# Kernel optimization log

Hardware: AMD Instinct MI355X
Metric: run time of the kernel (lower is better)

Reference implementation:

```python
import jax, jax.numpy as jnp
import numpy as np

DIM = 2048
N_HEADS = 16
HEAD_DIM = DIM // N_HEADS
MAX_SEQ_LEN = 2048
THRESHOLD = 0.7
LN_EPS = 1e-5


def _layernorm(x, g, b):
    mu = jnp.mean(x, axis=-1, keepdims=True)
    var = jnp.mean(jnp.square(x - mu), axis=-1, keepdims=True)
    return (x - mu) * jax.lax.rsqrt(var + LN_EPS) * g + b


def _act_quant(x):
    # 8-bit absmax activation quantization (per-tensor), straight-through
    s = 127.0 / jnp.maximum(jnp.max(jnp.abs(x)), 1e-5)
    xq = jnp.clip(jnp.round(x * s), -128.0, 127.0) / s
    return x + jax.lax.stop_gradient(xq - x)


def _ternary_quant(w):
    # W1.58 ternary: zero weights below threshold*mean|w|, scale = mean |w| over survivors
    delta = THRESHOLD * jnp.mean(jnp.abs(w))
    mask = (jnp.abs(w) > delta).astype(w.dtype)
    alpha = jnp.sum(jnp.abs(w) * mask) / jnp.maximum(jnp.sum(mask), 1.0)
    wq = jnp.sign(w) * mask * alpha
    return w + jax.lax.stop_gradient(wq - w)


def _bitlinear(x, w, g, b):
    x = _layernorm(x, g, b)
    xq = _act_quant(x)
    wq = _ternary_quant(w)
    return xq @ wq.T


def _rope_tables():
    inv = 1.0 / (10000.0 ** (np.arange(0, HEAD_DIM, 2, dtype=np.float32) / HEAD_DIM))
    t = np.arange(MAX_SEQ_LEN, dtype=np.float32)
    ang = np.outer(t, inv)  # (max_seq, head_dim/2)
    return jnp.asarray(np.cos(ang)), jnp.asarray(np.sin(ang))


def _apply_rope(x, cos_t, sin_t):
    # Faithful to source: x is (B, H, S, D) and freqs are indexed by x.shape[1] == H
    n = x.shape[1]
    xr = x.reshape(*x.shape[:-1], HEAD_DIM // 2, 2)
    a, b = xr[..., 0], xr[..., 1]
    c = cos_t[:n][None, :, None, :]  # (1, H, 1, D/2)
    s = sin_t[:n][None, :, None, :]
    out = jnp.stack([a * c - b * s, a * s + b * c], axis=-1)
    return out.reshape(x.shape)


def setup_inputs() -> dict:
    key = jax.random.key(0)
    ks = jax.random.split(key, 5)
    std = np.sqrt(2.0 / DIM)
    d = {"x": jax.random.normal(ks[0], (2, MAX_SEQ_LEN, DIM), dtype=jnp.float32)}
    for i, nm in enumerate(["q", "k", "v", "o"]):
        d[f"w_{nm}"] = jax.random.normal(ks[i + 1], (DIM, DIM), dtype=jnp.float32) * std
        d[f"g_{nm}"] = jnp.ones((DIM,), dtype=jnp.float32)
        d[f"b_{nm}"] = jnp.zeros((DIM,), dtype=jnp.float32)
    return d


def reference(x, w_q, g_q, b_q, w_k, g_k, b_k, w_v, g_v, b_v, w_o, g_o, b_o):
    B, S, _ = x.shape
    cos_t, sin_t = _rope_tables()
    scale = HEAD_DIM ** -0.5

    def split_heads(t):
        return t.reshape(B, S, N_HEADS, HEAD_DIM).transpose(0, 2, 1, 3)

    q = split_heads(_bitlinear(x, w_q, g_q, b_q))
    k = split_heads(_bitlinear(x, w_k, g_k, b_k))
    v = split_heads(_bitlinear(x, w_v, g_v, b_v))
    q = _apply_rope(q, cos_t, sin_t)
    k = _apply_rope(k, cos_t, sin_t)
    scores = jnp.einsum("bhsd,bhtd->bhst", q, k) * scale
    attn = jax.nn.softmax(scores, axis=-1)
    out = jnp.einsum("bhst,bhtd->bhsd", attn, v)
    out = out.transpose(0, 2, 1, 3).reshape(B, S, DIM)
    return _bitlinear(out, w_o, g_o, b_o)
```

## Files before the change

### kernel.cpp

```cpp
#include <hip/hip_runtime.h>
#include <math.h>

#define DIM 2048
#define NROWS 4096
#define WN (DIM*DIM)
#define HEADS 16
#define HDIM 128
#define SEQ 2048

typedef __attribute__((ext_vector_type(8))) short short8;
typedef __attribute__((ext_vector_type(8))) _Float16 half8;
typedef __attribute__((ext_vector_type(4))) float floatx4;
typedef __attribute__((ext_vector_type(4))) int intx4;

__device__ __forceinline__ unsigned short f2h(float f) {
  _Float16 h = (_Float16)f;
  return __builtin_bit_cast(unsigned short, h);
}
__device__ __forceinline__ float h2f(unsigned short u) {
  _Float16 h = __builtin_bit_cast(_Float16, u);
  return (float)h;
}

__device__ __forceinline__ void gload_lds16(const void* g, void* l) {
  __builtin_amdgcn_global_load_lds(
      (const __attribute__((address_space(1))) unsigned int*)g,
      (__attribute__((address_space(3))) unsigned int*)l, 16, 0, 0);
}

__device__ __forceinline__ float wredSum(float v) {
  #pragma unroll
  for (int o = 1; o < 64; o <<= 1) v += __shfl_xor(v, o);
  return v;
}
__device__ __forceinline__ float wredMax(float v) {
  #pragma unroll
  for (int o = 1; o < 64; o <<= 1) v = fmaxf(v, __shfl_xor(v, o));
  return v;
}

__device__ __forceinline__ float blockReduceSum(float v, float* red) {
  int tid = threadIdx.x;
  red[tid] = v; __syncthreads();
  for (int s = 128; s > 0; s >>= 1) {
    if (tid < s) red[tid] += red[tid + s];
    __syncthreads();
  }
  float r = red[0]; __syncthreads();
  return r;
}

__device__ __forceinline__ const float* pick_w(const float* a, const float* b,
                                               const float* c, const float* d, int i) {
  return i == 0 ? a : i == 1 ? b : i == 2 ? c : d;
}

__global__ __launch_bounds__(256) void w_abs_partial(
    const float* w0, const float* w1, const float* w2, const float* w3, float* part)
{
  const float4* w4 = (const float4*)pick_w(w0, w1, w2, w3, blockIdx.y);
  float s = 0.f;
  for (int i = blockIdx.x * 256 + threadIdx.x; i < WN / 4; i += 1024 * 256) {
    float4 v = w4[i];
    s += fabsf(v.x) + fabsf(v.y) + fabsf(v.z) + fabsf(v.w);
  }
  __shared__ float red[256];
  float t = blockReduceSum(s, red);
  if (threadIdx.x == 0) part[blockIdx.y * 1024 + blockIdx.x] = t;
}

__global__ __launch_bounds__(256) void w_delta_final(const float* part, float* stats)
{
  float s = 0.f;
  for (int i = threadIdx.x; i < 1024; i += 256) s += part[blockIdx.x * 1024 + i];
  __shared__ float red[256];
  float t = blockReduceSum(s, red);
  if (threadIdx.x == 0) stats[blockIdx.x] = 0.7f * (t / (float)WN);
}

__device__ __forceinline__ signed char tq(float v, float delta) {
  if (fabsf(v) > delta) return (v > 0.f) ? (signed char)1 : (signed char)-1;
  return (signed char)0;
}

__global__ __launch_bounds__(256) void w_maskquant(
    const float* w0, const float* w1, const float* w2, const float* w3,
    const float* stats, float* part2, signed char* tern)
{
  int wi = blockIdx.y;
  const float4* w4 = (const float4*)pick_w(w0, w1, w2, w3, wi);
  float delta = stats[wi];
  char4* out = (char4*)(tern + (size_t)wi * WN);
  float s = 0.f, cnt = 0.f;
  for (int i = blockIdx.x * 256 + threadIdx.x; i < WN / 4; i += 1024 * 256) {
    float4 v = w4[i];
    char4 o;
    float a;
    a = fabsf(v.x); if (a > delta) { s += a; cnt += 1.f; } o.x = tq(v.x, delta);
    a = fabsf(v.y); if (a > delta) { s += a; cnt += 1.f; } o.y = tq(v.y, delta);
    a = fabsf(v.z); if (a > delta) { s += a; cnt += 1.f; } o.z = tq(v.z, delta);
    a = fabsf(v.w); if (a > delta) { s += a; cnt += 1.f; } o.w = tq(v.w, delta);
    out[i] = o;
  }
  __shared__ float red[256];
  float ts = blockReduceSum(s, red);
  float tc = blockReduceSum(cnt, red);
  if (threadIdx.x == 0) {
    part2[((size_t)blockIdx.y * 1024 + blockIdx.x) * 2]     = ts;
    part2[((size_t)blockIdx.y * 1024 + blockIdx.x) * 2 + 1] = tc;
  }
}

__global__ __launch_bounds__(256) void w_alpha_final(const float* part2, float* stats)
{
  float s = 0.f, c = 0.f;
  for (int i = threadIdx.x; i < 1024; i += 256) {
    s += part2[((size_t)blockIdx.x * 1024 + i) * 2];
    c += part2[((size_t)blockIdx.x * 1024 + i) * 2 + 1];
  }
  __shared__ float red[256];
  float ts = blockReduceSum(s, red);
  float tc = blockReduceSum(c, red);
  if (threadIdx.x == 0) stats[4 + blockIdx.x] = ts / fmaxf(tc, 1.f);
}

__global__ __launch_bounds__(256) void ln_absmax3(
    const float* __restrict__ x,
    const float* __restrict__ g0, const float* __restrict__ b0,
    const float* __restrict__ g1, const float* __restrict__ b1,
    const float* __restrict__ g2, const float* __restrict__ b2,
    float* __restrict__ pmax)
{
  const int lane = threadIdx.x & 63;
  const int row = blockIdx.x * 4 + (threadIdx.x >> 6);
  const float* xr = x + (size_t)row * DIM;
  float4 a[8];
  float s = 0.f, sq = 0.f;
  #pragma unroll
  for (int j = 0; j < 8; ++j) {
    a[j] = *(const float4*)(xr + j * 256 + lane * 4);
    s  += a[j].x + a[j].y + a[j].z + a[j].w;
    sq += a[j].x*a[j].x + a[j].y*a[j].y + a[j].z*a[j].z + a[j].w*a[j].w;
  }
  s = wredSum(s); sq = wredSum(sq);
  float mu = s * (1.f / DIM);
  float var = sq * (1.f / DIM) - mu * mu;
  float rstd = 1.f / sqrtf(var + 1e-5f);
  const float* gs[3] = {g0, g1, g2};
  const float* bs[3] = {b0, b1, b2};
  #pragma unroll
  for (int p = 0; p < 3; ++p) {
    float m = 0.f;
    #pragma unroll
    for (int j = 0; j < 8; ++j) {
      float4 gg = *(const float4*)(gs[p] + j * 256 + lane * 4);
      float4 bb = *(const float4*)(bs[p] + j * 256 + lane * 4);
      m = fmaxf(m, fabsf((a[j].x - mu) * rstd * gg.x + bb.x));
      m = fmaxf(m, fabsf((a[j].y - mu) * rstd * gg.y + bb.y));
      m = fmaxf(m, fabsf((a[j].z - mu) * rstd * gg.z + bb.z));
      m = fmaxf(m, fabsf((a[j].w - mu) * rstd * gg.w + bb.w));
    }
    m = wredMax(m);
    if (lane == 0) pmax[(size_t)p * NROWS + row] = m;
  }
}

__global__ __launch_bounds__(256) void absmax_final(
    const float* __restrict__ pmax, unsigned* __restrict__ ambits)
{
  const float* src = pmax + (size_t)blockIdx.x * NROWS;
  float m = 0.f;
  for (int i = threadIdx.x; i < NROWS; i += 256) m = fmaxf(m, src[i]);
  m = wredMax(m);
  __shared__ float red[4];
  if ((threadIdx.x & 63) == 0) red[threadIdx.x >> 6] = m;
  __syncthreads();
  if (threadIdx.x == 0)
    ambits[blockIdx.x] = __float_as_uint(fmaxf(fmaxf(red[0], red[1]), fmaxf(red[2], red[3])));
}

__global__ __launch_bounds__(256) void ln_quant3(
    const float* __restrict__ x,
    const float* __restrict__ g0, const float* __restrict__ b0,
    const float* __restrict__ g1, const float* __restrict__ b1,
    const float* __restrict__ g2, const float* __restrict__ b2,
    const unsigned* __restrict__ ambits,
    signed char* __restrict__ xq0, signed char* __restrict__ xq1,
    signed char* __restrict__ xq2)
{
  const int lane = threadIdx.x & 63;
  const int row = blockIdx.x * 4 + (threadIdx.x >> 6);
  const float* xr = x + (size_t)row * DIM;
  float4 a[8];
  float s = 0.f, sq = 0.f;
  #pragma unroll
  for (int j = 0; j < 8; ++j) {
    a[j] = *(const float4*)(xr + j * 256 + lane * 4);
    s  += a[j].x + a[j].y + a[j].z + a[j].w;
    sq += a[j].x*a[j].x + a[j].y*a[j].y + a[j].z*a[j].z + a[j].w*a[j].w;
  }
  s = wredSum(s); sq = wredSum(sq);
  float mu = s * (1.f / DIM);
  float var = sq * (1.f / DIM) - mu * mu;
  float rstd = 1.f / sqrtf(var + 1e-5f);
  const float* gs[3] = {g0, g1, g2};
  const float* bs[3] = {b0, b1, b2};
  signed char* outs[3] = {xq0, xq1, xq2};
  #pragma unroll
  for (int p = 0; p < 3; ++p) {
    float sc = 127.f / fmaxf(__uint_as_float(ambits[p]), 1e-5f);
    #pragma unroll
    for (int j = 0; j < 8; ++j) {
      float4 gg = *(const float4*)(gs[p] + j * 256 + lane * 4);
      float4 bb = *(const float4*)(bs[p] + j * 256 + lane * 4);
      float y0 = (a[j].x - mu) * rstd * gg.x + bb.x;
      float y1 = (a[j].y - mu) * rstd * gg.y + bb.y;
      float y2 = (a[j].z - mu) * rstd * gg.z + bb.z;
      float y3 = (a[j].w - mu) * rstd * gg.w + bb.w;
      char4 q;
      q.x = (signed char)(int)fminf(fmaxf(rintf(y0 * sc), -128.f), 127.f);
      q.y = (signed char)(int)fminf(fmaxf(rintf(y1 * sc), -128.f), 127.f);
      q.z = (signed char)(int)fminf(fmaxf(rintf(y2 * sc), -128.f), 127.f);
      q.w = (signed char)(int)fminf(fmaxf(rintf(y3 * sc), -128.f), 127.f);
      *(char4*)(outs[p] + (size_t)row * DIM + j * 256 + lane * 4) = q;
    }
  }
}

template<int MODE>
__global__ __launch_bounds__(256) void ln_kernel(
    const float* __restrict__ x, const float* __restrict__ g, const float* __restrict__ bias,
    const unsigned* __restrict__ ambits, float* __restrict__ pmax,
    signed char* __restrict__ xq)
{
  const int lane = threadIdx.x & 63;
  const int row = blockIdx.x * 4 + (threadIdx.x >> 6);
  const float* xr = x + (size_t)row * DIM;
  float4 a[8];
  float s = 0.f, sq = 0.f;
  #pragma unroll
  for (int j = 0; j < 8; ++j) {
    a[j] = *(const float4*)(xr + j * 256 + lane * 4);
    s  += a[j].x + a[j].y + a[j].z + a[j].w;
    sq += a[j].x*a[j].x + a[j].y*a[j].y + a[j].z*a[j].z + a[j].w*a[j].w;
  }
  s = wredSum(s); sq = wredSum(sq);
  float mu = s * (1.f / DIM);
  float var = sq * (1.f / DIM) - mu * mu;
  float rstd = 1.f / sqrtf(var + 1e-5f);
  if (MODE == 0) {
    float m = 0.f;
    #pragma unroll
    for (int j = 0; j < 8; ++j) {
      float4 gg = *(const float4*)(g + j * 256 + lane * 4);
      float4 bb = *(const float4*)(bias + j * 256 + lane * 4);
      m = fmaxf(m, fabsf((a[j].x - mu) * rstd * gg.x + bb.x));
      m = fmaxf(m, fabsf((a[j].y - mu) * rstd * gg.y + bb.y));
      m = fmaxf(m, fabsf((a[j].z - mu) * rstd * gg.z + bb.z));
      m = fmaxf(m, fabsf((a[j].w - mu) * rstd * gg.w + bb.w));
    }
    m = wredMax(m);
    if (lane == 0) pmax[row] = m;
  } else {
    float sc = 127.f / fmaxf(__uint_as_float(*ambits), 1e-5f);
    #pragma unroll
    for (int j = 0; j < 8; ++j) {
      float4 gg = *(const float4*)(g + j * 256 + lane * 4);
      float4 bb = *(const float4*)(bias + j * 256 + lane * 4);
      float y0 = (a[j].x - mu) * rstd * gg.x + bb.x;
      float y1 = (a[j].y - mu) * rstd * gg.y + bb.y;
      float y2 = (a[j].z - mu) * rstd * gg.z + bb.z;
      float y3 = (a[j].w - mu) * rstd * gg.w + bb.w;
      char4 q;
      q.x = (signed char)(int)fminf(fmaxf(rintf(y0 * sc), -128.f), 127.f);
      q.y = (signed char)(int)fminf(fmaxf(rintf(y1 * sc), -128.f), 127.f);
      q.z = (signed char)(int)fminf(fmaxf(rintf(y2 * sc), -128.f), 127.f);
      q.w = (signed char)(int)fminf(fmaxf(rintf(y3 * sc), -128.f), 127.f);
      *(char4*)(xq + (size_t)row * DIM + j * 256 + lane * 4) = q;
    }
  }
}

__global__ __launch_bounds__(256) void gemm_qkv(
    const signed char* __restrict__ A0, const signed char* __restrict__ A1,
    const signed char* __restrict__ A2, const signed char* __restrict__ Bt0,
    unsigned short* __restrict__ C0, unsigned short* __restrict__ C1,
    unsigned short* __restrict__ C2t, const float* __restrict__ stats)
{
  const int tid = threadIdx.x;
  const int lane = tid & 63;
  const int w = tid >> 6;
  const int wm = w >> 1, wn = w & 1;
  const int quad = lane >> 4, l16 = lane & 15;
  const int bm = blockIdx.x * 128, bn = blockIdx.y * 128;
  const int z = blockIdx.z;

  const signed char* A  = z == 0 ? A0 : z == 1 ? A1 : A2;
  const signed char* Bt = Bt0 + (size_t)z * WN;

  __shared__ __align__(16) signed char smem[2 * 128 * 128];
  signed char* As = smem;
  signed char* Bs = smem + 128 * 128;

  const int srow_off = lane >> 3;
  const int scol     = (lane & 7) * 16;

  intx4 acc[4][4];
  #pragma unroll
  for (int i = 0; i < 4; ++i)
    #pragma unroll
    for (int j = 0; j < 4; ++j) acc[i][j] = {0, 0, 0, 0};

  for (int k0 = 0; k0 < DIM; k0 += 128) {
    #pragma unroll
    for (int i = 0; i < 4; ++i) {
      int c = i * 4 + w;
      int row = c * 8 + srow_off;
      gload_lds16(A  + (size_t)(bm + row) * DIM + k0 + scol, &As[c * 1024]);
      gload_lds16(Bt + (size_t)(bn + row) * DIM + k0 + scol, &Bs[c * 1024]);
    }
    __syncthreads();
    #pragma unroll
    for (int kc = 0; kc < 2; ++kc) {
      intx4 af[4], bf[4];
      #pragma unroll
      for (int i = 0; i < 4; ++i)
        af[i] = *(const intx4*)&As[(wm * 64 + i * 16 + l16) * 128 + kc * 64 + quad * 16];
      #pragma unroll
      for (int j = 0; j < 4; ++j)
        bf[j] = *(const intx4*)&Bs[(wn * 64 + j * 16 + l16) * 128 + kc * 64 + quad * 16];
      #pragma unroll
      for (int i = 0; i < 4; ++i)
        #pragma unroll
        for (int j = 0; j < 4; ++j)
          acc[i][j] = __builtin_amdgcn_mfma_i32_16x16x64_i8(af[i], bf[j], acc[i][j], 0, 0, 0);
    }
    __syncthreads();
  }

  const unsigned* am = (const unsigned*)(stats + 8);
  float scale = stats[4 + z] * fmaxf(__uint_as_float(am[z]), 1e-5f) * (1.f / 127.f);

  if (z < 2) {
    unsigned short* Cp = z == 0 ? C0 : C1;
    #pragma unroll
    for (int i = 0; i < 4; ++i)
      #pragma unroll
      for (int j = 0; j < 4; ++j)
        #pragma unroll
        for (int r = 0; r < 4; ++r) {
          int m = bm + wm * 64 + i * 16 + quad * 4 + r;
          int n = bn + wn * 64 + j * 16 + l16;
          Cp[(size_t)m * DIM + n] = f2h((float)acc[i][j][r] * scale);
        }
  } else {
    #pragma unroll
    for (int i = 0; i < 4; ++i)
      #pragma unroll
      for (int j = 0; j < 4; ++j)
        #pragma unroll
        for (int r = 0; r < 4; ++r) {
          int s = wm * 64 + i * 16 + quad * 4 + r;
          int d = wn * 64 + j * 16 + l16;
          int byte = (d * 256 + s * 2) ^ ((d & 7) << 4);
          *(unsigned short*)(smem + byte) = f2h((float)acc[i][j][r] * scale);
        }
    __syncthreads();
    const int b = bm >> 11;
    const int s_base = bm & (SEQ - 1);
    const int h = blockIdx.y;
    const int sc = (tid & 15) * 8;
    #pragma unroll
    for (int pass = 0; pass < 8; ++pass) {
      int d = (tid >> 4) + pass * 16;
      int byte = (d * 256 + sc * 2) ^ ((d & 7) << 4);
      *(uint4*)(C2t + ((size_t)(b * HEADS + h) * HDIM + d) * SEQ + s_base + sc) =
          *(const uint4*)(smem + byte);
    }
  }
}

__global__ __launch_bounds__(256) void gemm_bt(
    const signed char* __restrict__ A, const signed char* __restrict__ Bt,
    float* __restrict__ Cp, const float* __restrict__ stats, int wi)
{
  const int tid = threadIdx.x;
  const int lane = tid & 63;
  const int w = tid >> 6;
  const int wm = w >> 1, wn = w & 1;
  const int quad = lane >> 4, l16 = lane & 15;
  const int bm = blockIdx.x * 128, bn = blockIdx.y * 128;

  __shared__ __align__(16) signed char As[128 * 128];
  __shared__ __align__(16) signed char Bs[128 * 128];

  const int srow_off = lane >> 3;
  const int scol     = (lane & 7) * 16;

  intx4 acc[4][4];
  #pragma unroll
  for (int i = 0; i < 4; ++i)
    #pragma unroll
    for (int j = 0; j < 4; ++j) acc[i][j] = {0, 0, 0, 0};

  for (int k0 = 0; k0 < DIM; k0 += 128) {
    #pragma unroll
    for (int i = 0; i < 4; ++i) {
      int c = i * 4 + w;
      int row = c * 8 + srow_off;
      gload_lds16(A  + (size_t)(bm + row) * DIM + k0 + scol, &As[c * 1024]);
      gload_lds16(Bt + (size_t)(bn + row) * DIM + k0 + scol, &Bs[c * 1024]);
    }
    __syncthreads();
    #pragma unroll
    for (int kc = 0; kc < 2; ++kc) {
      intx4 af[4], bf[4];
      #pragma unroll
      for (int i = 0; i < 4; ++i)
        af[i] = *(const intx4*)&As[(wm * 64 + i * 16 + l16) * 128 + kc * 64 + quad * 16];
      #pragma unroll
      for (int j = 0; j < 4; ++j)
        bf[j] = *(const intx4*)&Bs[(wn * 64 + j * 16 + l16) * 128 + kc * 64 + quad * 16];
      #pragma unroll
      for (int i = 0; i < 4; ++i)
        #pragma unroll
        for (int j = 0; j < 4; ++j)
          acc[i][j] = __builtin_amdgcn_mfma_i32_16x16x64_i8(af[i], bf[j], acc[i][j], 0, 0, 0);
    }
    __syncthreads();
  }

  const unsigned* am = (const unsigned*)(stats + 8);
  float scale = stats[4 + wi] * fmaxf(__uint_as_float(am[wi]), 1e-5f) * (1.f / 127.f);
  #pragma unroll
  for (int i = 0; i < 4; ++i)
    #pragma unroll
    for (int j = 0; j < 4; ++j)
      #pragma unroll
      for (int r = 0; r < 4; ++r) {
        int m = bm + wm * 64 + i * 16 + quad * 4 + r;
        int n = bn + wn * 64 + j * 16 + l16;
        Cp[(size_t)m * DIM + n] = (float)acc[i][j][r] * scale;
      }
}

__global__ __launch_bounds__(256) void rope_kernel(unsigned short* q, unsigned short* k)
{
  const float SC = 0.12751741769011063f;
  int idx = blockIdx.x * 256 + threadIdx.x;
  int p = idx & 63;
  int h = (idx >> 6) & (HEADS - 1);
  int r = idx >> 10;
  float inv = exp2f((float)p * -0.20762050593046f);
  float ang = (float)h * inv;
  float sn, cs;
  __sincosf(ang, &sn, &cs);
  size_t base = (size_t)r * DIM + h * HDIM + 2 * p;
  {
    float a = h2f(q[base]), b = h2f(q[base + 1]);
    q[base]     = f2h((a * cs - b * sn) * SC);
    q[base + 1] = f2h((a * sn + b * cs) * SC);
  }
  {
    float a = h2f(k[base]), b = h2f(k[base + 1]);
    k[base]     = f2h(a * cs - b * sn);
    k[base + 1] = f2h(a * sn + b * cs);
  }
}

__global__ __launch_bounds__(256, 4) void flash_attn(
    const unsigned short* __restrict__ qf, const unsigned short* __restrict__ kf,
    const unsigned short* __restrict__ vt, float* __restrict__ o)
{
  const int tid = threadIdx.x;
  const int lane = tid & 63;
  const int w = tid >> 6;
  const int quad = lane >> 4;
  const int l16 = lane & 15;
  const int L = blockIdx.x;
  const int slot = L >> 3;
  const int bh = ((L & 7) << 2) | (slot >> 5);
  const int qt = slot & 31;
  const int b = bh >> 4;
  const int h = bh & 15;

  __shared__ __align__(16) char Ks[64 * 256];
  __shared__ __align__(16) char Vs[128 * 128];
  __shared__ __align__(16) char Ps[4][16 * 128];

  const size_t qbase = ((size_t)(b * SEQ + qt * 64 + w * 16 + l16)) * DIM + h * HDIM;
  short8 qa[4];
  #pragma unroll
  for (int kc = 0; kc < 4; ++kc)
    qa[kc] = *(const short8*)(qf + qbase + kc * 32 + quad * 8);

  float m_q = -INFINITY;
  float l_q = 0.f;
  floatx4 accO[8];
  #pragma unroll
  for (int i = 0; i < 8; ++i) accO[i] = {0.f, 0.f, 0.f, 0.f};

  const char* kg = (const char*)(kf + (size_t)(b * SEQ) * DIM + h * HDIM);
  const char* vg = (const char*)(vt + (size_t)bh * HDIM * SEQ);

  int koff[4], voff[4];
  #pragma unroll
  for (int j = 0; j < 4; ++j) {
    int c = w * 4 + j;
    int rK = c * 4 + (lane >> 4);
    koff[j] = rK * (DIM * 2) + (((lane & 15) * 16) ^ ((rK & 7) << 4));
    int rV = c * 8 + (lane >> 3);
    voff[j] = rV * (SEQ * 2) + (((lane & 7) * 16) ^ ((rV & 7) << 4));
  }

  for (int kt = 0; kt < SEQ / 64; ++kt) {
    __syncthreads();
    const char* kgb = kg + (size_t)kt * 64 * DIM * 2;
    const char* vgb = vg + (size_t)kt * 128;
    #pragma unroll
    for (int j = 0; j < 4; ++j) {
      int c = w * 4 + j;
      gload_lds16(kgb + koff[j], &Ks[c * 1024]);
      gload_lds16(vgb + voff[j], &Vs[c * 1024]);
    }
    asm volatile("s_waitcnt vmcnt(0)" ::: "memory");
    __syncthreads();

    float sreg[4][4];
    __builtin_amdgcn_s_setprio(1);
    #pragma unroll
    for (int jt = 0; jt < 4; ++jt) {
      floatx4 a0 = {0.f, 0.f, 0.f, 0.f};
      #pragma unroll
      for (int kc = 0; kc < 4; ++kc) {
        int kr = jt * 16 + l16;
        short8 kb = *(const short8*)&Ks[(kr * 256 + kc * 64 + quad * 16) ^ ((kr & 7) << 4)];
        a0 = __builtin_amdgcn_mfma_f32_16x16x32_f16(
            __builtin_bit_cast(half8, kb), __builtin_bit_cast(half8, qa[kc]), a0, 0, 0, 0);
      }
      #pragma unroll
      for (int r = 0; r < 4; ++r) sreg[jt][r] = a0[r];
    }
    __builtin_amdgcn_s_setprio(0);

    float mx = sreg[0][0];
    #pragma unroll
    for (int jt = 0; jt < 4; ++jt)
      #pragma unroll
      for (int r = 0; r < 4; ++r) mx = fmaxf(mx, sreg[jt][r]);
    mx = fmaxf(mx, __shfl_xor(mx, 16));
    mx = fmaxf(mx, __shfl_xor(mx, 32));
    int need = !__all(mx <= m_q + 8.f);
    float mnew, alpha;
    if (need) {
      mnew = fmaxf(m_q, mx);
      alpha = exp2f(m_q - mnew);
      m_q = mnew;
    } else {
      mnew = m_q;
      alpha = 1.f;
    }
    float ssum = 0.f;
    #pragma unroll
    for (int jt = 0; jt < 4; ++jt) {
      ushort4 pk;
      float p0 = exp2f(sreg[jt][0] - mnew);
      float p1 = exp2f(sreg[jt][1] - mnew);
      float p2 = exp2f(sreg[jt][2] - mnew);
      float p3 = exp2f(sreg[jt][3] - mnew);
      pk.x = f2h(p0); pk.y = f2h(p1); pk.z = f2h(p2); pk.w = f2h(p3);
      ssum += (p0 + p1) + (p2 + p3);
      *(ushort4*)&Ps[w][(l16 * 128 + jt * 32 + quad * 8) ^ ((l16 & 7) << 4)] = pk;
    }
    ssum += __shfl_xor(ssum, 16);
    ssum += __shfl_xor(ssum, 32);
    l_q = l_q * alpha + ssum;
    if (need) {
      #pragma unroll
      for (int dt = 0; dt < 8; ++dt)
        #pragma unroll
        for (int r = 0; r < 4; ++r) accO[dt][r] *= alpha;
    }

    __builtin_amdgcn_s_setprio(1);
    #pragma unroll
    for (int kc = 0; kc < 2; ++kc) {
      short8 pf = *(const short8*)&Ps[w][(l16 * 128 + kc * 64 + quad * 16) ^ ((l16 & 7) << 4)];
      #pragma unroll
      for (int dt = 0; dt < 8; ++dt) {
        int vr = dt * 16 + l16;
        short8 vf = *(const short8*)&Vs[(vr * 128 + kc * 64 + quad * 16) ^ ((vr & 7) << 4)];
        accO[dt] = __builtin_amdgcn_mfma_f32_16x16x32_f16(
            __builtin_bit_cast(half8, vf), __builtin_bit_cast(half8, pf), accO[dt], 0, 0, 0);
      }
    }
    __builtin_amdgcn_s_setprio(0);
  }

  float invl = 1.0f / l_q;
  const size_t obase = (size_t)(b * SEQ + qt * 64 + w * 16 + l16) * DIM + h * HDIM;
  #pragma unroll
  for (int dt = 0; dt < 8; ++dt) {
    float4 ov;
    ov.x = accO[dt][0] * invl; ov.y = accO[dt][1] * invl;
    ov.z = accO[dt][2] * invl; ov.w = accO[dt][3] * invl;
    *(float4*)(o + obase + dt * 16 + quad * 4) = ov;
  }
}

extern "C" void kernel_launch(void* const* d_in, const int* in_sizes, int n_in,
                              void* d_out, int out_size, void* d_ws, size_t ws_size,
                              hipStream_t stream)
{
  (void)in_sizes; (void)n_in; (void)out_size; (void)ws_size;
  const float* x = (const float*)d_in[0];
  const float* w[4]; const float* g[4]; const float* bb[4];
  for (int i = 0; i < 4; ++i) {
    w[i]  = (const float*)d_in[1 + 3 * i];
    g[i]  = (const float*)d_in[2 + 3 * i];
    bb[i] = (const float*)d_in[3 + 3 * i];
  }

  char* base = (char*)d_ws;
  size_t off = 0;
  auto alloc = [&](size_t bytes) {
    char* p = base + off;
    off += (bytes + 255) & ~(size_t)255;
    return p;
  };
  const size_t ACTH = (size_t)NROWS * DIM * 2;
  const size_t ACT8 = (size_t)NROWS * DIM;
  float* stats          = (float*)alloc(64);
  float* part1          = (float*)alloc(4 * 1024 * sizeof(float));
  float* part2          = (float*)alloc(4 * 1024 * 2 * sizeof(float));
  float* pmax           = (float*)alloc((size_t)4 * NROWS * sizeof(float));
  signed char* tern     = (signed char*)alloc((size_t)4 * WN);
  signed char* xq0      = (signed char*)alloc(ACT8);
  signed char* xq1      = (signed char*)alloc(ACT8);
  signed char* xq2      = (signed char*)alloc(ACT8);
  unsigned short* qh    = (unsigned short*)alloc(ACTH);
  unsigned short* kh    = (unsigned short*)alloc(ACTH);
  unsigned short* vtb   = (unsigned short*)alloc(ACTH);
  float* oat            = (float*)alloc((size_t)NROWS * DIM * sizeof(float));
  signed char* xqo = xq0;
  unsigned* ambits = (unsigned*)(stats + 8);

  hipMemsetAsync(stats, 0, 64, stream);

  dim3 b256(256);
  w_abs_partial<<<dim3(1024, 4), b256, 0, stream>>>(w[0], w[1], w[2], w[3], part1);
  w_delta_final<<<4, b256, 0, stream>>>(part1, stats);
  w_maskquant<<<dim3(1024, 4), b256, 0, stream>>>(w[0], w[1], w[2], w[3], stats, part2, tern);
  w_alpha_final<<<4, b256, 0, stream>>>(part2, stats);

  ln_absmax3<<<NROWS / 4, b256, 0, stream>>>(x, g[0], bb[0], g[1], bb[1], g[2], bb[2], pmax);
  absmax_final<<<3, b256, 0, stream>>>(pmax, ambits);
  ln_quant3<<<NROWS / 4, b256, 0, stream>>>(x, g[0], bb[0], g[1], bb[1], g[2], bb[2], ambits,
                                            xq0, xq1, xq2);

  gemm_qkv<<<dim3(NROWS / 128, DIM / 128, 3), b256, 0, stream>>>(
      xq0, xq1, xq2, tern, qh, kh, vtb, stats);

  rope_kernel<<<NROWS * 1024 / 256, b256, 0, stream>>>(qh, kh);
  flash_attn<<<dim3(32 * 32), b256, 0, stream>>>(qh, kh, vtb, oat);

  ln_kernel<0><<<NROWS / 4, b256, 0, stream>>>(oat, g[3], bb[3], nullptr,
                                               pmax + (size_t)3 * NROWS, nullptr);
  absmax_final<<<1, b256, 0, stream>>>(pmax + (size_t)3 * NROWS, ambits + 3);
  ln_kernel<1><<<NROWS / 4, b256, 0, stream>>>(oat, g[3], bb[3], ambits + 3, nullptr, xqo);
  gemm_bt<<<dim3(NROWS / 128, DIM / 128), b256, 0, stream>>>(
      xqo, tern + (size_t)3 * WN, (float*)d_out, stats, 3);
}
```

Before: 442.6 us.

## Double query rows per flash-attention wave to reuse K/V tiles

Each wave now processes two 16-row query fragments (128 query rows per block), so every K and V fragment loaded from LDS feeds two MFMAs. The grid shrinks to 512 blocks and launch bounds drop to 2 blocks per CU to make room for the doubled accumulators and score registers. P is packed to fp16 with the packed round-toward-zero convert. The aim is to halve K/V global and LDS traffic per query row, at the cost of lower occupancy and fewer blocks to spread across the GPU.

```diff
diff --git a/kernel.cpp b/kernel.cpp
--- a/kernel.cpp
+++ b/kernel.cpp
@@ -20,6 +20,9 @@
 __device__ __forceinline__ float h2f(unsigned short u) {
   _Float16 h = __builtin_bit_cast(_Float16, u);
   return (float)h;
+}
+__device__ __forceinline__ unsigned pkh2(float a, float b) {
+  return __builtin_bit_cast(unsigned, __builtin_amdgcn_cvt_pkrtz(a, b));
 }
 
 __device__ __forceinline__ void gload_lds16(const void* g, void* l) {
@@ -468,7 +471,7 @@
   }
 }
 
-__global__ __launch_bounds__(256, 4) void flash_attn(
+__global__ __launch_bounds__(256, 2) void flash_attn(
     const unsigned short* __restrict__ qf, const unsigned short* __restrict__ kf,
     const unsigned short* __restrict__ vt, float* __restrict__ o)
 {
@@ -479,26 +482,28 @@
   const int l16 = lane & 15;
   const int L = blockIdx.x;
   const int slot = L >> 3;
-  const int bh = ((L & 7) << 2) | (slot >> 5);
-  const int qt = slot & 31;
+  const int bh = ((L & 7) << 2) | (slot >> 4);
+  const int qt = slot & 15;
   const int b = bh >> 4;
   const int h = bh & 15;
 
   __shared__ __align__(16) char Ks[64 * 256];
   __shared__ __align__(16) char Vs[128 * 128];
-  __shared__ __align__(16) char Ps[4][16 * 128];
-
-  const size_t qbase = ((size_t)(b * SEQ + qt * 64 + w * 16 + l16)) * DIM + h * HDIM;
-  short8 qa[4];
-  #pragma unroll
-  for (int kc = 0; kc < 4; ++kc)
-    qa[kc] = *(const short8*)(qf + qbase + kc * 32 + quad * 8);
-
-  float m_q = -INFINITY;
-  float l_q = 0.f;
-  floatx4 accO[8];
-  #pragma unroll
-  for (int i = 0; i < 8; ++i) accO[i] = {0.f, 0.f, 0.f, 0.f};
+  __shared__ __align__(16) char Ps[4][32 * 128];
+
+  const size_t qbase = ((size_t)(b * SEQ + qt * 128 + w * 32 + l16)) * DIM + h * HDIM;
+  short8 qa[2][4];
+  #pragma unroll
+  for (int f = 0; f < 2; ++f)
+    #pragma unroll
+    for (int kc = 0; kc < 4; ++kc)
+      qa[f][kc] = *(const short8*)(qf + qbase + (size_t)f * 16 * DIM + kc * 32 + quad * 8);
+
+  float m_q[2] = {-INFINITY, -INFINITY};
+  float l_q[2] = {0.f, 0.f};
+  floatx4 accO0[8], accO1[8];
+  #pragma unroll
+  for (int i = 0; i < 8; ++i) { accO0[i] = {0.f, 0.f, 0.f, 0.f}; accO1[i] = {0.f, 0.f, 0.f, 0.f}; }
 
   const char* kg = (const char*)(kf + (size_t)(b * SEQ) * DIM + h * HDIM);
   const char* vg = (const char*)(vt + (size_t)bh * HDIM * SEQ);
@@ -526,85 +531,105 @@
     asm volatile("s_waitcnt vmcnt(0)" ::: "memory");
     __syncthreads();
 
-    float sreg[4][4];
+    float sreg[2][4][4];
     __builtin_amdgcn_s_setprio(1);
     #pragma unroll
     for (int jt = 0; jt < 4; ++jt) {
-      floatx4 a0 = {0.f, 0.f, 0.f, 0.f};
+      floatx4 a0 = {0.f, 0.f, 0.f, 0.f}, a1 = {0.f, 0.f, 0.f, 0.f};
       #pragma unroll
       for (int kc = 0; kc < 4; ++kc) {
         int kr = jt * 16 + l16;
         short8 kb = *(const short8*)&Ks[(kr * 256 + kc * 64 + quad * 16) ^ ((kr & 7) << 4)];
         a0 = __builtin_amdgcn_mfma_f32_16x16x32_f16(
-            __builtin_bit_cast(half8, kb), __builtin_bit_cast(half8, qa[kc]), a0, 0, 0, 0);
+            __builtin_bit_cast(half8, kb), __builtin_bit_cast(half8, qa[0][kc]), a0, 0, 0, 0);
+        a1 = __builtin_amdgcn_mfma_f32_16x16x32_f16(
+            __builtin_bit_cast(half8, kb), __builtin_bit_cast(half8, qa[1][kc]), a1, 0, 0, 0);
       }
       #pragma unroll
-      for (int r = 0; r < 4; ++r) sreg[jt][r] = a0[r];
+      for (int r = 0; r < 4; ++r) { sreg[0][jt][r] = a0[r]; sreg[1][jt][r] = a1[r]; }
     }
     __builtin_amdgcn_s_setprio(0);
 
-    float mx = sreg[0][0];
-    #pragma unroll
-    for (int jt = 0; jt < 4; ++jt)
-      #pragma unroll
-      for (int r = 0; r < 4; ++r) mx = fmaxf(mx, sreg[jt][r]);
-    mx = fmaxf(mx, __shfl_xor(mx, 16));
-    mx = fmaxf(mx, __shfl_xor(mx, 32));
-    int need = !__all(mx <= m_q + 8.f);
-    float mnew, alpha;
-    if (need) {
-      mnew = fmaxf(m_q, mx);
-      alpha = exp2f(m_q - mnew);
-      m_q = mnew;
-    } else {
-      mnew = m_q;
-      alpha = 1.f;
-    }
-    float ssum = 0.f;
-    #pragma unroll
-    for (int jt = 0; jt < 4; ++jt) {
-      ushort4 pk;
-      float p0 = exp2f(sreg[jt][0] - mnew);
-      float p1 = exp2f(sreg[jt][1] - mnew);
-      float p2 = exp2f(sreg[jt][2] - mnew);
-      float p3 = exp2f(sreg[jt][3] - mnew);
-      pk.x = f2h(p0); pk.y = f2h(p1); pk.z = f2h(p2); pk.w = f2h(p3);
-      ssum += (p0 + p1) + (p2 + p3);
-      *(ushort4*)&Ps[w][(l16 * 128 + jt * 32 + quad * 8) ^ ((l16 & 7) << 4)] = pk;
-    }
-    ssum += __shfl_xor(ssum, 16);
-    ssum += __shfl_xor(ssum, 32);
-    l_q = l_q * alpha + ssum;
-    if (need) {
+    float alpha[2]; int need[2];
+    #pragma unroll
+    for (int f = 0; f < 2; ++f) {
+      float mx = sreg[f][0][0];
+      #pragma unroll
+      for (int jt = 0; jt < 4; ++jt)
+        #pragma unroll
+        for (int r = 0; r < 4; ++r) mx = fmaxf(mx, sreg[f][jt][r]);
+      mx = fmaxf(mx, __shfl_xor(mx, 16));
+      mx = fmaxf(mx, __shfl_xor(mx, 32));
+      need[f] = !__all(mx <= m_q[f] + 8.f);
+      float mnew;
+      if (need[f]) {
+        mnew = fmaxf(m_q[f], mx);
+        alpha[f] = exp2f(m_q[f] - mnew);
+        m_q[f] = mnew;
+      } else {
+        mnew = m_q[f];
+        alpha[f] = 1.f;
+      }
+      float ssum = 0.f;
+      #pragma unroll
+      for (int jt = 0; jt < 4; ++jt) {
+        float p0 = exp2f(sreg[f][jt][0] - mnew);
+        float p1 = exp2f(sreg[f][jt][1] - mnew);
+        float p2 = exp2f(sreg[f][jt][2] - mnew);
+        float p3 = exp2f(sreg[f][jt][3] - mnew);
+        uint2 pk2;
+        pk2.x = pkh2(p0, p1);
+        pk2.y = pkh2(p2, p3);
+        ssum += (p0 + p1) + (p2 + p3);
+        *(uint2*)&Ps[w][((f * 16 + l16) * 128 + jt * 32 + quad * 8) ^ ((l16 & 7) << 4)] = pk2;
+      }
+      ssum += __shfl_xor(ssum, 16);
+      ssum += __shfl_xor(ssum, 32);
+      l_q[f] = l_q[f] * alpha[f] + ssum;
+    }
+    if (need[0]) {
       #pragma unroll
       for (int dt = 0; dt < 8; ++dt)
         #pragma unroll
-        for (int r = 0; r < 4; ++r) accO[dt][r] *= alpha;
+        for (int r = 0; r < 4; ++r) accO0[dt][r] *= alpha[0];
+    }
+    if (need[1]) {
+      #pragma unroll
+      for (int dt = 0; dt < 8; ++dt)
+        #pragma unroll
+        for (int r = 0; r < 4; ++r) accO1[dt][r] *= alpha[1];
     }
 
     __builtin_amdgcn_s_setprio(1);
     #pragma unroll
     for (int kc = 0; kc < 2; ++kc) {
-      short8 pf = *(const short8*)&Ps[w][(l16 * 128 + kc * 64 + quad * 16) ^ ((l16 & 7) << 4)];
+      short8 pf0 = *(const short8*)&Ps[w][(l16 * 128 + kc * 64 + quad * 16) ^ ((l16 & 7) << 4)];
+      short8 pf1 = *(const short8*)&Ps[w][((16 + l16) * 128 + kc * 64 + quad * 16) ^ ((l16 & 7) << 4)];
       #pragma unroll
       for (int dt = 0; dt < 8; ++dt) {
         int vr = dt * 16 + l16;
         short8 vf = *(const short8*)&Vs[(vr * 128 + kc * 64 + quad * 16) ^ ((vr & 7) << 4)];
-        accO[dt] = __builtin_amdgcn_mfma_f32_16x16x32_f16(
-            __builtin_bit_cast(half8, vf), __builtin_bit_cast(half8, pf), accO[dt], 0, 0, 0);
+        accO0[dt] = __builtin_amdgcn_mfma_f32_16x16x32_f16(
+            __builtin_bit_cast(half8, vf), __builtin_bit_cast(half8, pf0), accO0[dt], 0, 0, 0);
+        accO1[dt] = __builtin_amdgcn_mfma_f32_16x16x32_f16(
+            __builtin_bit_cast(half8, vf), __builtin_bit_cast(half8, pf1), accO1[dt], 0, 0, 0);
       }
     }
     __builtin_amdgcn_s_setprio(0);
   }
 
-  float invl = 1.0f / l_q;
-  const size_t obase = (size_t)(b * SEQ + qt * 64 + w * 16 + l16) * DIM + h * HDIM;
-  #pragma unroll
-  for (int dt = 0; dt < 8; ++dt) {
-    float4 ov;
-    ov.x = accO[dt][0] * invl; ov.y = accO[dt][1] * invl;
-    ov.z = accO[dt][2] * invl; ov.w = accO[dt][3] * invl;
-    *(float4*)(o + obase + dt * 16 + quad * 4) = ov;
+  #pragma unroll
+  for (int f = 0; f < 2; ++f) {
+    float invl = 1.0f / l_q[f];
+    const size_t obase = (size_t)(b * SEQ + qt * 128 + w * 32 + f * 16 + l16) * DIM + h * HDIM;
+    #pragma unroll
+    for (int dt = 0; dt < 8; ++dt) {
+      floatx4 acc = f == 0 ? accO0[dt] : accO1[dt];
+      float4 ov;
+      ov.x = acc[0] * invl; ov.y = acc[1] * invl;
+      ov.z = acc[2] * invl; ov.w = acc[3] * invl;
+      *(float4*)(o + obase + dt * 16 + quad * 4) = ov;
+    }
   }
 }
 
@@ -662,7 +687,7 @@
       xq0, xq1, xq2, tern, qh, kh, vtb, stats);
 
   rope_kernel<<<NROWS * 1024 / 256, b256, 0, stream>>>(qh, kh);
-  flash_attn<<<dim3(32 * 32), b256, 0, stream>>>(qh, kh, vtb, oat);
+  flash_attn<<<dim3(16 * 32), b256, 0, stream>>>(qh, kh, vtb, oat);
 
   ln_kernel<0><<<NROWS / 4, b256, 0, stream>>>(oat, g[3], bb[3], nullptr,
                                                pmax + (size_t)3 * NROWS, nullptr);
```

Result: faster. 429.8 us (-2.9%).
